# Kernel optimization log

Hardware: AMD Instinct MI355X
Metric: run time of the kernel (lower is better)

## Reference

```python
import jax, jax.numpy as jnp
import numpy as np

B, N, S, K = 8, 4096, 256, 128   # clouds, points/cloud, FPS samples (num_vote_test), neighbor cap
R = 0.2                           # ball-query radius
M = 45                            # FoldingNet grid side -> 45*45 = 2025 grid points


def _fps(pos):
    """Deterministic farthest point sampling of S points from pos [N,3] (start at index 0)."""
    n = pos.shape[0]
    big = jnp.finfo(pos.dtype).max

    def step(carry, _):
        mind, last = carry
        d = jnp.sum((pos - pos[last]) ** 2, axis=-1)
        mind = jnp.minimum(mind, d)
        nxt = jnp.argmax(mind).astype(jnp.int32)
        return (mind, nxt), nxt

    init = (jnp.full((n,), big, pos.dtype), jnp.int32(0))
    _, rest = jax.lax.scan(step, init, None, length=S - 1)
    return jnp.concatenate([jnp.zeros((1,), jnp.int32), rest])


def _forward(pos, Wt, bt, Wc1, bc1, Wc2, bc2, Wc3, bc3, We1, be1, We2, be2,
             Wf11, bf11, Wf12, bf12, Wf13, bf13, Wf21, bf21, Wf22, bf22, Wf23, bf23):
    lrelu = jax.nn.leaky_relu  # slope 0.01, matches torch LeakyReLU default
    # transformer: mlp([3,64]) -- BatchNorm at eval with default stats is identity
    x = lrelu(pos @ Wt + bt)                                  # [B,N,64]
    # FPS per cloud
    idx = jax.vmap(_fps)(pos)                                  # [B,S]
    new_pos = jnp.take_along_axis(pos, idx[..., None], axis=1)  # [B,S,3]
    # radius ball query: first K in-ball neighbors by index order (torch_cluster semantics)
    d2 = jnp.sum((new_pos[:, :, None, :] - pos[:, None, :, :]) ** 2, -1)  # [B,S,N]
    inball = d2 <= R * R
    keep = inball & (jnp.cumsum(inball, axis=-1) <= K)
    order = jnp.where(keep, jnp.arange(N)[None, None, :], N)
    nidx = jnp.sort(order, axis=-1)[..., :K]                   # [B,S,K]
    valid = nidx < N
    nsafe = jnp.minimum(nidx, N - 1)
    gather = jax.vmap(lambda a, i: a[i])
    xj = gather(x, nsafe)                                      # [B,S,K,64]
    pj = gather(pos, nsafe)                                    # [B,S,K,3]
    # PointConv: mlp(cat[x_j, pos_j - pos_i]) with max aggregation
    feat = jnp.concatenate([xj, pj - new_pos[:, :, None, :]], -1)  # [B,S,K,67]
    h = lrelu(feat @ Wc1 + bc1)
    h = lrelu(h @ Wc2 + bc2)
    h = lrelu(h @ Wc3 + bc3)                                   # [B,S,K,512]
    neg = jnp.finfo(h.dtype).min
    agg = jnp.max(jnp.where(valid[..., None], h, neg), axis=2)  # [B,S,512]
    # encoder mlp([515, 512, 2*bottleneck], last=True)
    e = lrelu(jnp.concatenate([agg, new_pos], -1) @ We1 + be1)
    e = e @ We2 + be2                                          # [B,S,2*bottleneck]
    mean, logvar = jnp.split(e, 2, axis=-1)
    std = jnp.exp(0.5 * logvar)
    # feature_selection (eval, rand=False): all S votes contribute; vote aggregation
    z = jnp.sum(mean / std, axis=1) / jnp.sum(1.0 / std, axis=1)  # [B,bottleneck]
    # FoldingNet decoder: 45x45 grid in [-0.3,0.3]^2, conv1x1 == last-dim linear
    g1 = np.linspace(-0.3, 0.3, M, dtype=np.float32)
    mg = np.meshgrid(g1, g1)
    grid = jnp.asarray(np.stack([mg[0].reshape(-1), mg[1].reshape(-1)], -1))  # [M*M,2]
    G = M * M
    code = jnp.broadcast_to(z[:, None, :], (z.shape[0], G, z.shape[1]))
    gb = jnp.broadcast_to(grid[None], (z.shape[0], G, 2))
    f = jnp.concatenate([code, gb], -1)                        # [B,G,bottleneck+2]
    f = jax.nn.relu(f @ Wf11 + bf11)
    f = jax.nn.relu(f @ Wf12 + bf12)
    f = f @ Wf13 + bf13                                        # [B,G,3]
    f2 = jnp.concatenate([code, f], -1)                        # [B,G,bottleneck+3]
    f2 = jax.nn.relu(f2 @ Wf21 + bf21)
    f2 = jax.nn.relu(f2 @ Wf22 + bf22)
    return f2 @ Wf23 + bf23                                    # [B,G,3]


_PARAM_SHAPES = [
    ("Wt", (3, 64)), ("bt", (64,)),
    ("Wc1", (67, 64)), ("bc1", (64,)),
    ("Wc2", (64, 128)), ("bc2", (128,)),
    ("Wc3", (128, 512)), ("bc3", (512,)),
    ("We1", (515, 512)), ("be1", (512,)),
    ("We2", (512, 2048)), ("be2", (2048,)),
    ("Wf11", (1026, 512)), ("bf11", (512,)),
    ("Wf12", (512, 512)), ("bf12", (512,)),
    ("Wf13", (512, 3)), ("bf13", (3,)),
    ("Wf21", (1027, 512)), ("bf21", (512,)),
    ("Wf22", (512, 512)), ("bf22", (512,)),
    ("Wf23", (512, 3)), ("bf23", (3,)),
]


def setup_inputs() -> dict:
    key = jax.random.key(0)
    inp = {"pos": jax.random.uniform(key, (B, N, 3), jnp.float32)}
    for i, (nm, sh) in enumerate(_PARAM_SHAPES):
        k = jax.random.fold_in(key, i + 1)
        fan_in = sh[0]
        inp[nm] = jax.random.normal(k, sh, jnp.float32) / np.sqrt(fan_in)
    return inp


def reference(pos, Wt, bt, Wc1, bc1, Wc2, bc2, Wc3, bc3, We1, be1, We2, be2,
              Wf11, bf11, Wf12, bf12, Wf13, bf13, Wf21, bf21, Wf22, bf22, Wf23, bf23):
    return _forward(pos, Wt, bt, Wc1, bc1, Wc2, bc2, Wc3, bc3, We1, be1, We2, be2,
                    Wf11, bf11, Wf12, bf12, Wf13, bf13, Wf21, bf21, Wf22, bf22, Wf23, bf23)
```

## Files before the change

### kernel.cpp

```cpp
#include <hip/hip_runtime.h>
#include <math.h>

#define BATCH 8
#define NPTS 4096
#define SSAMP 256
#define KNBR 128
#define GGRID 2025

typedef __attribute__((ext_vector_type(8))) short bf16x8;
typedef __attribute__((ext_vector_type(8))) unsigned short u16x8;
typedef __attribute__((ext_vector_type(4))) float f32x4;
#define MFMA16(a, b, c) __builtin_amdgcn_mfma_f32_16x16x32_bf16((a), (b), (c), 0, 0, 0)

__device__ __forceinline__ float lrelu01(float v) { return v > 0.f ? v : 0.01f * v; }
__device__ __forceinline__ unsigned short f2bf(float f) {
    unsigned u = __float_as_uint(f);
    unsigned r = (u + 0x7FFFu + ((u >> 16) & 1u)) >> 16;
    return (unsigned short)r;
}
__device__ __forceinline__ unsigned long long umax64(unsigned long long a, unsigned long long b) {
    return a > b ? a : b;
}

__global__ void preconv_kernel(const float* __restrict__ Wc1, const float* __restrict__ Wc2,
                               const float* __restrict__ Wc3, const float* __restrict__ We1,
                               const float* __restrict__ We2, const float* __restrict__ Wf12,
                               const float* __restrict__ Wf22,
                               unsigned short* __restrict__ W1T, unsigned short* __restrict__ W2T,
                               unsigned short* __restrict__ W3T, unsigned short* __restrict__ We1T,
                               unsigned short* __restrict__ We2T, unsigned short* __restrict__ Wf12T,
                               unsigned short* __restrict__ Wf22T) {
    int o = blockIdx.x * 256 + threadIdx.x;
    const int S1 = 6144, S2 = 8192, S3 = 65536, S4 = 294912, S5 = 1048576, S6 = 262144;
    if (o < S1) { int n = o / 96, k = o - n * 96; W1T[o] = f2bf(k < 67 ? Wc1[k * 64 + n] : 0.f); return; }
    o -= S1;
    if (o < S2) { int n = o >> 6, k = o & 63; W2T[o] = f2bf(Wc2[k * 128 + n]); return; }
    o -= S2;
    if (o < S3) { int n = o >> 7, k = o & 127; W3T[o] = f2bf(Wc3[k * 512 + n]); return; }
    o -= S3;
    if (o < S4) { int n = o / 576, k = o - n * 576; We1T[o] = f2bf(k < 515 ? We1[k * 512 + n] : 0.f); return; }
    o -= S4;
    if (o < S5) { int n = o >> 9, k = o & 511; We2T[o] = f2bf(We2[k * 2048 + n]); return; }
    o -= S5;
    if (o < S6) { int n = o >> 9, k = o & 511; Wf12T[o] = f2bf(Wf12[k * 512 + n]); return; }
    o -= S6;
    { int n = o >> 9, k = o & 511; Wf22T[o] = f2bf(Wf22[k * 512 + n]); }
}

__global__ void __launch_bounds__(256, 3) stage1_kernel(
    const float* __restrict__ pos, float* __restrict__ newpos, int* __restrict__ prog,
    const float* __restrict__ Wt, const float* __restrict__ bt,
    const unsigned short* __restrict__ W1T, const unsigned short* __restrict__ W2T,
    const unsigned short* __restrict__ W3T,
    const float* __restrict__ bc1, const float* __restrict__ bc2, const float* __restrict__ bc3,
    unsigned short* __restrict__ encin) {
    __shared__ __align__(16) unsigned char smem[53760];
    int blk = blockIdx.x, t = threadIdx.x;
    int wave = t >> 6, lane = t & 63;

    if (blk < 8) {
        float* pxs = (float*)smem;
        float* pys = (float*)(smem + 16384);
        float* pzs = (float*)(smem + 32768);
        float* npb = (float*)(smem + 49152);
        unsigned long long* rk = (unsigned long long*)(smem + 52224);
        int b = blk;
        const float* P = pos + (size_t)b * NPTS * 3;
        float* np = newpos + (size_t)b * SSAMP * 3;
        float px[16], py[16], pz[16], mind[16];
#pragma unroll
        for (int j = 0; j < 16; ++j) {
            int n = t + 256 * j;
            float X = P[n * 3 + 0], Y = P[n * 3 + 1], Z = P[n * 3 + 2];
            px[j] = X; py[j] = Y; pz[j] = Z;
            pxs[n] = X; pys[n] = Y; pzs[n] = Z;
            mind[j] = 3.402823466e+38f;
        }
        float cx = P[0], cy = P[1], cz = P[2];
        if (t == 0) { npb[0] = cx; npb[1] = cy; npb[2] = cz; }
        __syncthreads();
        for (int s = 1; s < SSAMP; ++s) {
            int p = s & 1;
            unsigned long long k[16];
#pragma unroll
            for (int j = 0; j < 16; ++j) {
                float dx = __fsub_rn(px[j], cx), dy = __fsub_rn(py[j], cy), dz = __fsub_rn(pz[j], cz);
                float d = __fadd_rn(__fadd_rn(__fmul_rn(dx, dx), __fmul_rn(dy, dy)), __fmul_rn(dz, dz));
                mind[j] = fminf(mind[j], d);
                k[j] = ((unsigned long long)__float_as_uint(mind[j]) << 32)
                     | (unsigned)~(unsigned)(t + 256 * j);
            }
#pragma unroll
            for (int st = 8; st > 0; st >>= 1)
#pragma unroll
                for (int j = 0; j < st; ++j) k[j] = umax64(k[j], k[j + st]);
            unsigned long long key = k[0];
            {
                unsigned long long a = __shfl_xor(key, 1, 64);
                unsigned long long b2 = __shfl_xor(key, 2, 64);
                unsigned long long c = __shfl_xor(key, 3, 64);
                key = umax64(umax64(key, a), umax64(b2, c));
                a = __shfl_xor(key, 4, 64);
                b2 = __shfl_xor(key, 8, 64);
                c = __shfl_xor(key, 12, 64);
                key = umax64(umax64(key, a), umax64(b2, c));
                a = __shfl_xor(key, 16, 64);
                b2 = __shfl_xor(key, 32, 64);
                c = __shfl_xor(key, 48, 64);
                key = umax64(umax64(key, a), umax64(b2, c));
            }
            if (lane == 0) rk[p * 4 + wave] = key;
            __syncthreads();
            unsigned long long k0 = rk[p * 4 + 0], k1 = rk[p * 4 + 1];
            unsigned long long k2 = rk[p * 4 + 2], k3 = rk[p * 4 + 3];
            unsigned long long bk = umax64(umax64(k0, k1), umax64(k2, k3));
            int nx = (int)(~(unsigned)(bk & 0xFFFFFFFFull));
            cx = pxs[nx]; cy = pys[nx]; cz = pzs[nx];
            if (t == 0) {
                npb[s * 3 + 0] = cx;
                npb[s * 3 + 1] = cy;
                npb[s * 3 + 2] = cz;
            }
            if ((s & 7) == 7) {
                if (t < 24) np[(s - 7) * 3 + t] = npb[(s - 7) * 3 + t];
                if (t == 0) {
                    __threadfence();
                    __hip_atomic_store(&prog[b], s, __ATOMIC_RELAXED, __HIP_MEMORY_SCOPE_AGENT);
                }
            }
        }
        return;
    }

    unsigned short* featl = (unsigned short*)smem;
    unsigned short* h2    = (unsigned short*)smem;
    unsigned short* h1    = (unsigned short*)(smem + 34816);
    float* mred = (float*)(smem + 34816);
    int*   vld  = (int*)(smem + 53248);
    int*   wl   = (int*)smem;
    int*   cnt  = (int*)(smem + 2048);
    float* wtb  = (float*)(smem + 26624);

    int cons = blk - 8;
    int s = cons >> 3, b = cons & 7;
    int bs = b * 256 + s;
    int quad = lane >> 4, l16 = lane & 15;

    if (t == 0) {
        while (__hip_atomic_load(&prog[b], __ATOMIC_RELAXED, __HIP_MEMORY_SCOPE_AGENT) < s)
            __builtin_amdgcn_s_sleep(16);
    }
    __syncthreads();
    __threadfence();
    float q0 = newpos[(size_t)bs * 3 + 0];
    float q1 = newpos[(size_t)bs * 3 + 1];
    float q2 = newpos[(size_t)bs * 3 + 2];

    const float* P = pos + (size_t)b * NPTS * 3;
    {
        int base = 0;
        for (int c = 0; c < 16 && base < KNBR; ++c) {
            int n = wave * 1024 + c * 64 + lane;
            float dx = __fsub_rn(P[n * 3 + 0], q0);
            float dy = __fsub_rn(P[n * 3 + 1], q1);
            float dz = __fsub_rn(P[n * 3 + 2], q2);
            float d2 = __fadd_rn(__fadd_rn(__fmul_rn(dx, dx), __fmul_rn(dy, dy)), __fmul_rn(dz, dz));
            bool in = (d2 <= 0.04f);
            unsigned long long mask = __ballot(in);
            if (in) {
                int p = base + __popcll(mask & ((1ull << lane) - 1ull));
                if (p < KNBR) wl[wave * 128 + p] = n;
            }
            base += __popcll(mask);
        }
        if (lane == 0) cnt[wave] = base < KNBR ? base : KNBR;
    }
    __syncthreads();
    {
        int c0 = cnt[0], c1 = cnt[1], c2 = cnt[2], c3 = cnt[3];
        if (t < 128) {
            int idx = -1, r = t;
            if (r < c0) idx = wl[r];
            else {
                r -= c0;
                if (r < c1) idx = wl[128 + r];
                else {
                    r -= c1;
                    if (r < c2) idx = wl[256 + r];
                    else { r -= c2; if (r < c3) idx = wl[384 + r]; }
                }
            }
            vld[t] = idx;
        }
        if (t < 192) wtb[t] = Wt[t];
        else wtb[t] = bt[t - 192];
    }
    __syncthreads();

    int vbits = 0;
#pragma unroll
    for (int i = 0; i < 2; ++i)
#pragma unroll
        for (int reg = 0; reg < 4; ++reg)
            if (vld[(2 * wave + i) * 16 + quad * 4 + reg] >= 0) vbits |= 1 << (i * 4 + reg);

    {
        int sr = t >> 1, sh = t & 1;
        int n = vld[sr];
        int ns = n < 0 ? 0 : n;
        const float* pp = pos + ((size_t)b * NPTS + ns) * 3;
        float p0 = pp[0], p1 = pp[1], p2 = pp[2];
        unsigned short* frow = &featl[sr * 104];
        u16x8 z8 = {0, 0, 0, 0, 0, 0, 0, 0};
        if (n >= 0) {
#pragma unroll
            for (int g = 0; g < 4; ++g) {
                u16x8 v8;
#pragma unroll
                for (int e = 0; e < 8; ++e) {
                    int c = sh * 32 + g * 8 + e;
                    float v = fmaf(p2, wtb[128 + c], fmaf(p1, wtb[64 + c], fmaf(p0, wtb[c], wtb[192 + c])));
                    v8[e] = (unsigned short)f2bf(lrelu01(v));
                }
                *(u16x8*)&frow[sh * 32 + g * 8] = v8;
            }
        } else {
#pragma unroll
            for (int g = 0; g < 4; ++g) *(u16x8*)&frow[sh * 32 + g * 8] = z8;
        }
        if (sh == 1) {
            u16x8 dv = z8;
            if (n >= 0) {
                dv[0] = (unsigned short)f2bf(__fsub_rn(p0, q0));
                dv[1] = (unsigned short)f2bf(__fsub_rn(p1, q1));
                dv[2] = (unsigned short)f2bf(__fsub_rn(p2, q2));
            }
            *(u16x8*)&frow[64] = dv;
            *(u16x8*)&frow[72] = z8;
            *(u16x8*)&frow[80] = z8;
            *(u16x8*)&frow[88] = z8;
        }
    }
    __syncthreads();

    {
        f32x4 acc[2][4];
#pragma unroll
        for (int i = 0; i < 2; ++i)
#pragma unroll
            for (int nt = 0; nt < 4; ++nt) acc[i][nt] = (f32x4){0.f, 0.f, 0.f, 0.f};
#pragma unroll
        for (int ks = 0; ks < 3; ++ks) {
            bf16x8 afr[2];
#pragma unroll
            for (int i = 0; i < 2; ++i)
                afr[i] = *(const bf16x8*)&featl[((2 * wave + i) * 16 + l16) * 104 + ks * 32 + quad * 8];
#pragma unroll
            for (int nt = 0; nt < 4; ++nt) {
                bf16x8 bfr = *(const bf16x8*)(W1T + (nt * 16 + l16) * 96 + ks * 32 + quad * 8);
                acc[0][nt] = MFMA16(afr[0], bfr, acc[0][nt]);
                acc[1][nt] = MFMA16(afr[1], bfr, acc[1][nt]);
            }
        }
#pragma unroll
        for (int i = 0; i < 2; ++i)
#pragma unroll
            for (int nt = 0; nt < 4; ++nt) {
                int col = nt * 16 + l16;
                float bias = bc1[col];
#pragma unroll
                for (int reg = 0; reg < 4; ++reg) {
                    int row = (2 * wave + i) * 16 + quad * 4 + reg;
                    h1[row * 72 + col] = f2bf(lrelu01(acc[i][nt][reg] + bias));
                }
            }
    }
    __syncthreads();

    {
        f32x4 acc[2][8];
#pragma unroll
        for (int i = 0; i < 2; ++i)
#pragma unroll
            for (int nt = 0; nt < 8; ++nt) acc[i][nt] = (f32x4){0.f, 0.f, 0.f, 0.f};
#pragma unroll
        for (int ks = 0; ks < 2; ++ks) {
            bf16x8 afr[2];
#pragma unroll
            for (int i = 0; i < 2; ++i)
                afr[i] = *(const bf16x8*)&h1[((2 * wave + i) * 16 + l16) * 72 + ks * 32 + quad * 8];
#pragma unroll
            for (int nt = 0; nt < 8; ++nt) {
                bf16x8 bfr = *(const bf16x8*)(W2T + (nt * 16 + l16) * 64 + ks * 32 + quad * 8);
                acc[0][nt] = MFMA16(afr[0], bfr, acc[0][nt]);
                acc[1][nt] = MFMA16(afr[1], bfr, acc[1][nt]);
            }
        }
        __syncthreads();
#pragma unroll
        for (int i = 0; i < 2; ++i)
#pragma unroll
            for (int nt = 0; nt < 8; ++nt) {
                int col = nt * 16 + l16;
                float bias = bc2[col];
#pragma unroll
                for (int reg = 0; reg < 4; ++reg) {
                    int row = (2 * wave + i) * 16 + quad * 4 + reg;
                    h2[row * 136 + col] = f2bf(lrelu01(acc[i][nt][reg] + bias));
                }
            }
    }
    __syncthreads();

    for (int c3 = 0; c3 < 4; ++c3) {
        f32x4 acc[2][8];
#pragma unroll
        for (int i = 0; i < 2; ++i)
#pragma unroll
            for (int nt = 0; nt < 8; ++nt) acc[i][nt] = (f32x4){0.f, 0.f, 0.f, 0.f};
#pragma unroll
        for (int ks = 0; ks < 4; ++ks) {
            bf16x8 afr[2];
#pragma unroll
            for (int i = 0; i < 2; ++i)
                afr[i] = *(const bf16x8*)&h2[((2 * wave + i) * 16 + l16) * 136 + ks * 32 + quad * 8];
#pragma unroll
            for (int nt = 0; nt < 8; ++nt) {
                bf16x8 bfr = *(const bf16x8*)(W3T + ((size_t)((c3 * 8 + nt) * 16 + l16)) * 128 + ks * 32 + quad * 8);
                acc[0][nt] = MFMA16(afr[0], bfr, acc[0][nt]);
                acc[1][nt] = MFMA16(afr[1], bfr, acc[1][nt]);
            }
        }
#pragma unroll
        for (int nt = 0; nt < 8; ++nt) {
            float vmax = -3.402823466e+38f;
#pragma unroll
            for (int i = 0; i < 2; ++i)
#pragma unroll
                for (int reg = 0; reg < 4; ++reg)
                    if (vbits & (1 << (i * 4 + reg))) vmax = fmaxf(vmax, acc[i][nt][reg]);
            vmax = fmaxf(vmax, __shfl_xor(vmax, 16));
            vmax = fmaxf(vmax, __shfl_xor(vmax, 32));
            if (lane < 16) mred[wave * 512 + (c3 * 8 + nt) * 16 + l16] = vmax;
        }
    }
    __syncthreads();
    unsigned short* erow = encin + (size_t)bs * 576;
    for (int c = t; c < 576; c += 256) {
        unsigned short v;
        if (c < 512) {
            float m4 = fmaxf(fmaxf(mred[c], mred[512 + c]), fmaxf(mred[1024 + c], mred[1536 + c]));
            v = f2bf(lrelu01(m4 + bc3[c]));
        } else if (c < 515) {
            v = f2bf(c == 512 ? q0 : (c == 513 ? q1 : q2));
        } else v = 0;
        erow[c] = v;
    }
}

__global__ void __launch_bounds__(256, 3) mfma_gemm(
    const unsigned short* __restrict__ A, const unsigned short* __restrict__ BT,
    const float* __restrict__ bias, float* __restrict__ outf, unsigned short* __restrict__ outh,
    int M, int Ka, int Ncols, int act) {
    __shared__ __align__(16) unsigned short As[128 * 72];
    int t = threadIdx.x;
    int wave = t >> 6, lane = t & 63, quad = lane >> 4, l16 = lane & 15;
    int row0 = blockIdx.x * 128, col0 = blockIdx.y * 128;
    f32x4 acc[2][8];
#pragma unroll
    for (int i = 0; i < 2; ++i)
#pragma unroll
        for (int nt = 0; nt < 8; ++nt) acc[i][nt] = (f32x4){0.f, 0.f, 0.f, 0.f};
    int nk = Ka >> 6;
    int sr = t >> 1, sh = t & 1;
    int grow = row0 + sr; if (grow > M - 1) grow = M - 1;
    const unsigned short* Arow = A + (size_t)grow * Ka + sh * 32;
    for (int ks = 0; ks < nk; ++ks) {
        u16x8 av[4];
#pragma unroll
        for (int j = 0; j < 4; ++j) av[j] = *(const u16x8*)(Arow + ks * 64 + j * 8);
        __syncthreads();
#pragma unroll
        for (int j = 0; j < 4; ++j) *(u16x8*)&As[sr * 72 + sh * 32 + j * 8] = av[j];
        __syncthreads();
#pragma unroll
        for (int ks2 = 0; ks2 < 2; ++ks2) {
            bf16x8 afr[2];
            afr[0] = *(const bf16x8*)&As[((2 * wave) * 16 + l16) * 72 + ks2 * 32 + quad * 8];
            afr[1] = *(const bf16x8*)&As[((2 * wave + 1) * 16 + l16) * 72 + ks2 * 32 + quad * 8];
#pragma unroll
            for (int nt = 0; nt < 8; ++nt) {
                bf16x8 bfr = *(const bf16x8*)(BT + (size_t)(col0 + nt * 16 + l16) * Ka + ks * 64 + ks2 * 32 + quad * 8);
                acc[0][nt] = MFMA16(afr[0], bfr, acc[0][nt]);
                acc[1][nt] = MFMA16(afr[1], bfr, acc[1][nt]);
            }
        }
    }
#pragma unroll
    for (int i = 0; i < 2; ++i)
#pragma unroll
        for (int nt = 0; nt < 8; ++nt) {
            int col = col0 + nt * 16 + l16;
            float bv = bias[col];
#pragma unroll
            for (int reg = 0; reg < 4; ++reg) {
                int row = row0 + (2 * wave + i) * 16 + quad * 4 + reg;
                if (row < M) {
                    float v = acc[i][nt][reg] + bv;
                    if (act == 1) v = fmaxf(v, 0.f);
                    else if (act == 2) v = lrelu01(v);
                    if (outh) outh[(size_t)row * Ncols + col] = f2bf(v);
                    else outf[(size_t)row * Ncols + col] = v;
                }
            }
        }
}

__global__ void __launch_bounds__(256) votes_kernel(const float* __restrict__ e, float* __restrict__ z) {
    __shared__ float red[8][32][2];
    int blk = blockIdx.x;
    int b = blk >> 5, c0 = (blk & 31) << 5;
    int t = threadIdx.x, c = t & 31, sg = t >> 5;
    const float* eb = e + (size_t)b * SSAMP * 2048;
    float num = 0.f, den = 0.f;
    for (int si = 0; si < 32; ++si) {
        int s = sg * 32 + si;
        float mean = eb[(size_t)s * 2048 + c0 + c];
        float lv = eb[(size_t)s * 2048 + 1024 + c0 + c];
        float sd = expf(0.5f * lv);
        num += mean / sd;
        den += 1.f / sd;
    }
    red[sg][c][0] = num; red[sg][c][1] = den;
    __syncthreads();
    if (sg == 0) {
        float n = 0.f, d = 0.f;
#pragma unroll
        for (int k = 0; k < 8; ++k) { n += red[k][c][0]; d += red[k][c][1]; }
        z[b * 1024 + c0 + c] = n / d;
    }
}

__global__ void __launch_bounds__(256) ukern(const float* __restrict__ z,
                                             const float* __restrict__ Wf11, const float* __restrict__ bf11,
                                             const float* __restrict__ Wf21, const float* __restrict__ bf21,
                                             float* __restrict__ u1, float* __restrict__ u2) {
    __shared__ float zt[1024 * 8];
    __shared__ float red[4][64][8];
    const float* W = blockIdx.y ? Wf21 : Wf11;
    const float* bias = blockIdx.y ? bf21 : bf11;
    float* u = blockIdx.y ? u2 : u1;
    int t = threadIdx.x;
#pragma unroll
    for (int i = 0; i < 32; ++i) {
        int o = t + i * 256;
        zt[(o & 1023) * 8 + (o >> 10)] = z[o];
    }
    __syncthreads();
    int c64 = t & 63, kc = t >> 6;
    int co = blockIdx.x * 64 + c64;
    float acc[8];
#pragma unroll
    for (int r = 0; r < 8; ++r) acc[r] = 0.f;
    for (int i = 0; i < 256; ++i) {
        int ci = kc * 256 + i;
        float w = W[(size_t)ci * 512 + co];
        const float4* zp = (const float4*)&zt[ci * 8];
        float4 z0 = zp[0], z1 = zp[1];
        acc[0] = fmaf(z0.x, w, acc[0]); acc[1] = fmaf(z0.y, w, acc[1]);
        acc[2] = fmaf(z0.z, w, acc[2]); acc[3] = fmaf(z0.w, w, acc[3]);
        acc[4] = fmaf(z1.x, w, acc[4]); acc[5] = fmaf(z1.y, w, acc[5]);
        acc[6] = fmaf(z1.z, w, acc[6]); acc[7] = fmaf(z1.w, w, acc[7]);
    }
#pragma unroll
    for (int r = 0; r < 8; ++r) red[kc][c64][r] = acc[r];
    __syncthreads();
    if (kc == 0) {
#pragma unroll
        for (int r = 0; r < 8; ++r) {
            float v = red[0][c64][r] + red[1][c64][r] + red[2][c64][r] + red[3][c64][r] + bias[co];
            u[r * 512 + co] = v;
        }
    }
}

__global__ void fold1_kernel(const float* __restrict__ u1, const float* __restrict__ Wf11,
                             unsigned short* __restrict__ f1) {
    int o = blockIdx.x * 256 + threadIdx.x;
    int co = o & 511;
    int rg = o >> 9;
    int b = rg / 2025;
    int g = rg - b * 2025;
    int i = g / 45, j = g - i * 45;
    float gx = (j == 44) ? 0.3f : (float)(-0.3 + j * (0.6 / 44.0));
    float gy = (i == 44) ? 0.3f : (float)(-0.3 + i * (0.6 / 44.0));
    float v = u1[(b << 9) + co];
    v = fmaf(gx, Wf11[1024 * 512 + co], v);
    v = fmaf(gy, Wf11[1025 * 512 + co], v);
    f1[o] = f2bf(fmaxf(v, 0.f));
}

__global__ void fold2_kernel(const float* __restrict__ u2, const float* __restrict__ Wf21,
                             const float* __restrict__ pts, unsigned short* __restrict__ f2) {
    int o = blockIdx.x * 256 + threadIdx.x;
    int co = o & 511;
    int rg = o >> 9;
    int b = rg / 2025;
    float p0 = pts[rg * 3 + 0], p1 = pts[rg * 3 + 1], p2 = pts[rg * 3 + 2];
    float v = u2[(b << 9) + co];
    v = fmaf(p0, Wf21[1024 * 512 + co], v);
    v = fmaf(p1, Wf21[1025 * 512 + co], v);
    v = fmaf(p2, Wf21[1026 * 512 + co], v);
    f2[o] = f2bf(fmaxf(v, 0.f));
}

__global__ void smallout_kernel(const unsigned short* __restrict__ H, const float* __restrict__ Wf,
                                const float* __restrict__ bf, float* __restrict__ out, int rows) {
    int rg = blockIdx.x * 256 + threadIdx.x;
    if (rg >= rows) return;
    const unsigned int* h = (const unsigned int*)(H + (size_t)rg * 512);
    float a0 = bf[0], a1 = bf[1], a2 = bf[2];
#pragma unroll 4
    for (int q = 0; q < 256; ++q) {
        unsigned int p = h[q];
        float e0 = __uint_as_float(p << 16);
        float e1 = __uint_as_float(p & 0xFFFF0000u);
        int k = q * 2;
        a0 = fmaf(e0, Wf[k * 3 + 0], a0);
        a1 = fmaf(e0, Wf[k * 3 + 1], a1);
        a2 = fmaf(e0, Wf[k * 3 + 2], a2);
        a0 = fmaf(e1, Wf[k * 3 + 3], a0);
        a1 = fmaf(e1, Wf[k * 3 + 4], a1);
        a2 = fmaf(e1, Wf[k * 3 + 5], a2);
    }
    out[rg * 3 + 0] = a0;
    out[rg * 3 + 1] = a1;
    out[rg * 3 + 2] = a2;
}

extern "C" void kernel_launch(void* const* d_in, const int* in_sizes, int n_in,
                              void* d_out, int out_size, void* d_ws, size_t ws_size,
                              hipStream_t stream) {
    const float* pos  = (const float*)d_in[0];
    const float* Wt   = (const float*)d_in[1];
    const float* bt   = (const float*)d_in[2];
    const float* Wc1  = (const float*)d_in[3];
    const float* bc1  = (const float*)d_in[4];
    const float* Wc2  = (const float*)d_in[5];
    const float* bc2  = (const float*)d_in[6];
    const float* Wc3  = (const float*)d_in[7];
    const float* bc3  = (const float*)d_in[8];
    const float* We1  = (const float*)d_in[9];
    const float* be1  = (const float*)d_in[10];
    const float* We2  = (const float*)d_in[11];
    const float* be2  = (const float*)d_in[12];
    const float* Wf11 = (const float*)d_in[13];
    const float* bf11 = (const float*)d_in[14];
    const float* Wf12 = (const float*)d_in[15];
    const float* bf12 = (const float*)d_in[16];
    const float* Wf13 = (const float*)d_in[17];
    const float* bf13 = (const float*)d_in[18];
    const float* Wf21 = (const float*)d_in[19];
    const float* bf21 = (const float*)d_in[20];
    const float* Wf22 = (const float*)d_in[21];
    const float* bf22 = (const float*)d_in[22];
    const float* Wf23 = (const float*)d_in[23];
    const float* bf23 = (const float*)d_in[24];
    float* out = (float*)d_out;

    float* wsf = (float*)d_ws;
    size_t off = 0;
    unsigned short* encinh= (unsigned short*)(wsf + off); off += 589824;
    unsigned short* e1h   = (unsigned short*)(wsf + off); off += 524288;
    float* e    = wsf + off; off += 4194304;
    unsigned short* f1h   = (unsigned short*)(wsf + off); off += 4147200;
    unsigned short* h12h  = (unsigned short*)(wsf + off); off += 4147200;
    float* zb   = wsf + off; off += 8192;
    float* u1   = wsf + off; off += 4096;
    float* u2   = wsf + off; off += 4096;
    float* pts  = wsf + off; off += 48600;
    float* newp = wsf + off; off += 6144;
    int*   prog = (int*)(wsf + off); off += 16;
    unsigned short* W1T   = (unsigned short*)(wsf + off); off += 3072;
    unsigned short* W2T   = (unsigned short*)(wsf + off); off += 4096;
    unsigned short* W3T   = (unsigned short*)(wsf + off); off += 32768;
    unsigned short* We1T  = (unsigned short*)(wsf + off); off += 147456;
    unsigned short* We2T  = (unsigned short*)(wsf + off); off += 524288;
    unsigned short* Wf12T = (unsigned short*)(wsf + off); off += 131072;
    unsigned short* Wf22T = (unsigned short*)(wsf + off); off += 131072;

    hipMemsetAsync(prog, 0xFF, 64, stream);
    preconv_kernel<<<7608, 256, 0, stream>>>(Wc1, Wc2, Wc3, We1, We2, Wf12, Wf22,
                                             W1T, W2T, W3T, We1T, We2T, Wf12T, Wf22T);
    stage1_kernel<<<2056, 256, 0, stream>>>(pos, newp, prog, Wt, bt, W1T, W2T, W3T,
                                            bc1, bc2, bc3, encinh);
    mfma_gemm<<<dim3(16, 4), 256, 0, stream>>>(encinh, We1T, be1, nullptr, e1h, 2048, 576, 512, 2);
    mfma_gemm<<<dim3(16, 16), 256, 0, stream>>>(e1h, We2T, be2, e, nullptr, 2048, 512, 2048, 0);
    votes_kernel<<<256, 256, 0, stream>>>(e, zb);
    ukern<<<dim3(8, 2), 256, 0, stream>>>(zb, Wf11, bf11, Wf21, bf21, u1, u2);
    fold1_kernel<<<32400, 256, 0, stream>>>(u1, Wf11, f1h);
    mfma_gemm<<<dim3(127, 4), 256, 0, stream>>>(f1h, Wf12T, bf12, nullptr, h12h, 16200, 512, 512, 1);
    smallout_kernel<<<64, 256, 0, stream>>>(h12h, Wf13, bf13, pts, 16200);
    fold2_kernel<<<32400, 256, 0, stream>>>(u2, Wf21, pts, f1h);
    mfma_gemm<<<dim3(127, 4), 256, 0, stream>>>(f1h, Wf22T, bf22, nullptr, h12h, 16200, 512, 512, 1);
    smallout_kernel<<<64, 256, 0, stream>>>(h12h, Wf23, bf23, out, 16200);
}
```

Baseline: 681.9 us.

## Fuse vote reduction into encoder GEMM and fold stages into single MFMA kernels

The second encoder GEMM now interleaves mean and log-variance columns in its weight layout so each lane pair can compute precision-weighted vote partial sums directly from accumulators. These sums go to global memory via atomics, which removes the fp32 intermediate and the separate votes kernel. Each folding stage (fold input build, 512x512 GEMM with ReLU, 512->3 projection) is fused into one kernel that builds the A tile on the fly and reduces the projection with shuffles, so the large bf16 intermediates are never written. The fold kernels launch only 127 blocks with a serial loop over four column chunks, which may leave the GPU underused. The atomics also make the vote sums order-nondeterministic.

```diff
diff --git a/kernel.cpp b/kernel.cpp
--- a/kernel.cpp
+++ b/kernel.cpp
@@ -40,7 +40,12 @@
     o -= S3;
     if (o < S4) { int n = o / 576, k = o - n * 576; We1T[o] = f2bf(k < 515 ? We1[k * 512 + n] : 0.f); return; }
     o -= S4;
-    if (o < S5) { int n = o >> 9, k = o & 511; We2T[o] = f2bf(We2[k * 2048 + n]); return; }
+    if (o < S5) {
+        int np = o >> 9, k = o & 511;
+        int src = (np & 1) ? 1024 + (np >> 1) : (np >> 1);
+        We2T[o] = f2bf(We2[(size_t)k * 2048 + src]);
+        return;
+    }
     o -= S5;
     if (o < S6) { int n = o >> 9, k = o & 511; Wf12T[o] = f2bf(Wf12[k * 512 + n]); return; }
     o -= S6;
@@ -360,7 +365,7 @@
 
 __global__ void __launch_bounds__(256, 3) mfma_gemm(
     const unsigned short* __restrict__ A, const unsigned short* __restrict__ BT,
-    const float* __restrict__ bias, float* __restrict__ outf, unsigned short* __restrict__ outh,
+    const float* __restrict__ bias, unsigned short* __restrict__ outh,
     int M, int Ka, int Ncols, int act) {
     __shared__ __align__(16) unsigned short As[128 * 72];
     int t = threadIdx.x;
@@ -409,39 +414,75 @@
                     float v = acc[i][nt][reg] + bv;
                     if (act == 1) v = fmaxf(v, 0.f);
                     else if (act == 2) v = lrelu01(v);
-                    if (outh) outh[(size_t)row * Ncols + col] = f2bf(v);
-                    else outf[(size_t)row * Ncols + col] = v;
-                }
-            }
-        }
-}
-
-__global__ void __launch_bounds__(256) votes_kernel(const float* __restrict__ e, float* __restrict__ z) {
-    __shared__ float red[8][32][2];
-    int blk = blockIdx.x;
-    int b = blk >> 5, c0 = (blk & 31) << 5;
-    int t = threadIdx.x, c = t & 31, sg = t >> 5;
-    const float* eb = e + (size_t)b * SSAMP * 2048;
-    float num = 0.f, den = 0.f;
-    for (int si = 0; si < 32; ++si) {
-        int s = sg * 32 + si;
-        float mean = eb[(size_t)s * 2048 + c0 + c];
-        float lv = eb[(size_t)s * 2048 + 1024 + c0 + c];
-        float sd = expf(0.5f * lv);
-        num += mean / sd;
-        den += 1.f / sd;
-    }
-    red[sg][c][0] = num; red[sg][c][1] = den;
-    __syncthreads();
-    if (sg == 0) {
-        float n = 0.f, d = 0.f;
-#pragma unroll
-        for (int k = 0; k < 8; ++k) { n += red[k][c][0]; d += red[k][c][1]; }
-        z[b * 1024 + c0 + c] = n / d;
-    }
-}
-
-__global__ void __launch_bounds__(256) ukern(const float* __restrict__ z,
+                    outh[(size_t)row * Ncols + col] = f2bf(v);
+                }
+            }
+        }
+}
+
+__global__ void __launch_bounds__(256, 3) e2v_kernel(
+    const unsigned short* __restrict__ A, const unsigned short* __restrict__ BT,
+    const float* __restrict__ be2, float* __restrict__ zacc) {
+    __shared__ __align__(16) unsigned short As[128 * 72];
+    int t = threadIdx.x;
+    int wave = t >> 6, lane = t & 63, quad = lane >> 4, l16 = lane & 15;
+    int row0 = blockIdx.x * 128, col0 = blockIdx.y * 128;
+    f32x4 acc[2][8];
+#pragma unroll
+    for (int i = 0; i < 2; ++i)
+#pragma unroll
+        for (int nt = 0; nt < 8; ++nt) acc[i][nt] = (f32x4){0.f, 0.f, 0.f, 0.f};
+    int sr = t >> 1, sh = t & 1;
+    const unsigned short* Arow = A + (size_t)(row0 + sr) * 512 + sh * 32;
+    for (int ks = 0; ks < 8; ++ks) {
+        u16x8 av[4];
+#pragma unroll
+        for (int j = 0; j < 4; ++j) av[j] = *(const u16x8*)(Arow + ks * 64 + j * 8);
+        __syncthreads();
+#pragma unroll
+        for (int j = 0; j < 4; ++j) *(u16x8*)&As[sr * 72 + sh * 32 + j * 8] = av[j];
+        __syncthreads();
+#pragma unroll
+        for (int ks2 = 0; ks2 < 2; ++ks2) {
+            bf16x8 afr[2];
+            afr[0] = *(const bf16x8*)&As[((2 * wave) * 16 + l16) * 72 + ks2 * 32 + quad * 8];
+            afr[1] = *(const bf16x8*)&As[((2 * wave + 1) * 16 + l16) * 72 + ks2 * 32 + quad * 8];
+#pragma unroll
+            for (int nt = 0; nt < 8; ++nt) {
+                bf16x8 bfr = *(const bf16x8*)(BT + (size_t)(col0 + nt * 16 + l16) * 512 + ks * 64 + ks2 * 32 + quad * 8);
+                acc[0][nt] = MFMA16(afr[0], bfr, acc[0][nt]);
+                acc[1][nt] = MFMA16(afr[1], bfr, acc[1][nt]);
+            }
+        }
+    }
+    int b = row0 >> 8;
+#pragma unroll
+    for (int nt = 0; nt < 8; ++nt) {
+        int colp = col0 + nt * 16 + l16;
+        int c2 = colp >> 1;
+        int srcc = (colp & 1) ? 1024 + c2 : c2;
+        float bv = be2[srcc];
+        float num = 0.f, den = 0.f;
+#pragma unroll
+        for (int i = 0; i < 2; ++i)
+#pragma unroll
+            for (int reg = 0; reg < 4; ++reg) {
+                float val = acc[i][nt][reg] + bv;
+                float par = __shfl_xor(val, 1, 64);
+                float d = expf(-0.5f * par);
+                num += val * d;
+                den += d;
+            }
+        num += __shfl_xor(num, 16, 64); den += __shfl_xor(den, 16, 64);
+        num += __shfl_xor(num, 32, 64); den += __shfl_xor(den, 32, 64);
+        if (quad == 0 && !(l16 & 1)) {
+            atomicAdd(&zacc[((b << 10) + c2) * 2 + 0], num);
+            atomicAdd(&zacc[((b << 10) + c2) * 2 + 1], den);
+        }
+    }
+}
+
+__global__ void __launch_bounds__(256) ukern(const float* __restrict__ zacc,
                                              const float* __restrict__ Wf11, const float* __restrict__ bf11,
                                              const float* __restrict__ Wf21, const float* __restrict__ bf21,
                                              float* __restrict__ u1, float* __restrict__ u2) {
@@ -451,10 +492,12 @@
     const float* bias = blockIdx.y ? bf21 : bf11;
     float* u = blockIdx.y ? u2 : u1;
     int t = threadIdx.x;
+    const float2* za = (const float2*)zacc;
 #pragma unroll
     for (int i = 0; i < 32; ++i) {
         int o = t + i * 256;
-        zt[(o & 1023) * 8 + (o >> 10)] = z[o];
+        float2 nd = za[o];
+        zt[(o & 1023) * 8 + (o >> 10)] = nd.x / nd.y;
     }
     __syncthreads();
     int c64 = t & 63, kc = t >> 6;
@@ -484,58 +527,128 @@
     }
 }
 
-__global__ void fold1_kernel(const float* __restrict__ u1, const float* __restrict__ Wf11,
-                             unsigned short* __restrict__ f1) {
-    int o = blockIdx.x * 256 + threadIdx.x;
-    int co = o & 511;
-    int rg = o >> 9;
-    int b = rg / 2025;
-    int g = rg - b * 2025;
-    int i = g / 45, j = g - i * 45;
-    float gx = (j == 44) ? 0.3f : (float)(-0.3 + j * (0.6 / 44.0));
-    float gy = (i == 44) ? 0.3f : (float)(-0.3 + i * (0.6 / 44.0));
-    float v = u1[(b << 9) + co];
-    v = fmaf(gx, Wf11[1024 * 512 + co], v);
-    v = fmaf(gy, Wf11[1025 * 512 + co], v);
-    f1[o] = f2bf(fmaxf(v, 0.f));
-}
-
-__global__ void fold2_kernel(const float* __restrict__ u2, const float* __restrict__ Wf21,
-                             const float* __restrict__ pts, unsigned short* __restrict__ f2) {
-    int o = blockIdx.x * 256 + threadIdx.x;
-    int co = o & 511;
-    int rg = o >> 9;
-    int b = rg / 2025;
-    float p0 = pts[rg * 3 + 0], p1 = pts[rg * 3 + 1], p2 = pts[rg * 3 + 2];
-    float v = u2[(b << 9) + co];
-    v = fmaf(p0, Wf21[1024 * 512 + co], v);
-    v = fmaf(p1, Wf21[1025 * 512 + co], v);
-    v = fmaf(p2, Wf21[1026 * 512 + co], v);
-    f2[o] = f2bf(fmaxf(v, 0.f));
-}
-
-__global__ void smallout_kernel(const unsigned short* __restrict__ H, const float* __restrict__ Wf,
-                                const float* __restrict__ bf, float* __restrict__ out, int rows) {
-    int rg = blockIdx.x * 256 + threadIdx.x;
-    if (rg >= rows) return;
-    const unsigned int* h = (const unsigned int*)(H + (size_t)rg * 512);
-    float a0 = bf[0], a1 = bf[1], a2 = bf[2];
-#pragma unroll 4
-    for (int q = 0; q < 256; ++q) {
-        unsigned int p = h[q];
-        float e0 = __uint_as_float(p << 16);
-        float e1 = __uint_as_float(p & 0xFFFF0000u);
-        int k = q * 2;
-        a0 = fmaf(e0, Wf[k * 3 + 0], a0);
-        a1 = fmaf(e0, Wf[k * 3 + 1], a1);
-        a2 = fmaf(e0, Wf[k * 3 + 2], a2);
-        a0 = fmaf(e1, Wf[k * 3 + 3], a0);
-        a1 = fmaf(e1, Wf[k * 3 + 4], a1);
-        a2 = fmaf(e1, Wf[k * 3 + 5], a2);
-    }
-    out[rg * 3 + 0] = a0;
-    out[rg * 3 + 1] = a1;
-    out[rg * 3 + 2] = a2;
+__global__ void __launch_bounds__(256, 3) foldfuse_kernel(
+    const float* __restrict__ u, const float* __restrict__ Wfold, int nExtra, int mode,
+    const unsigned short* __restrict__ WT, const float* __restrict__ bmid,
+    const float* __restrict__ wout, const float* __restrict__ bout,
+    const float* __restrict__ pts_in, float* __restrict__ outv) {
+    __shared__ __align__(16) unsigned short As[128 * 72];
+    __shared__ float sW[3][512];
+    __shared__ float sU[2][512];
+    __shared__ float sP[512 * 3];
+    __shared__ float sB[512];
+    __shared__ float sRC[128][4];
+    int t = threadIdx.x, wave = t >> 6, lane = t & 63, quad = lane >> 4, l16 = lane & 15;
+    int row0 = blockIdx.x * 128;
+    int b0 = row0 / 2025;
+
+    for (int idx = t; idx < 1536; idx += 256) {
+        int r = idx >> 9, c = idx & 511;
+        sW[r][c] = (r < nExtra) ? Wfold[(size_t)(1024 + r) * 512 + c] : 0.f;
+    }
+    for (int idx = t; idx < 1536; idx += 256) sP[idx] = wout[idx];
+    for (int idx = t; idx < 1024; idx += 256) {
+        int rb = idx >> 9;
+        int bb = b0 + rb; if (bb > 7) bb = 7;
+        sU[rb][idx & 511] = u[bb * 512 + (idx & 511)];
+    }
+    for (int idx = t; idx < 512; idx += 256) sB[idx] = bmid[idx];
+    if (t < 128) {
+        int rg = row0 + t; if (rg > 16199) rg = 16199;
+        int b = rg / 2025, g = rg - b * 2025;
+        if (mode == 0) {
+            int i = g / 45, j = g - i * 45;
+            sRC[t][0] = (j == 44) ? 0.3f : (float)(-0.3 + j * (0.6 / 44.0));
+            sRC[t][1] = (i == 44) ? 0.3f : (float)(-0.3 + i * (0.6 / 44.0));
+            sRC[t][2] = 0.f;
+        } else {
+            sRC[t][0] = pts_in[rg * 3 + 0];
+            sRC[t][1] = pts_in[rg * 3 + 1];
+            sRC[t][2] = pts_in[rg * 3 + 2];
+        }
+        sRC[t][3] = __int_as_float(b - b0);
+    }
+    __syncthreads();
+
+    float proj[2][4][3];
+#pragma unroll
+    for (int i = 0; i < 2; ++i)
+#pragma unroll
+        for (int r = 0; r < 4; ++r) { proj[i][r][0] = 0.f; proj[i][r][1] = 0.f; proj[i][r][2] = 0.f; }
+
+    int sr = t >> 1, sh = t & 1;
+    for (int cc = 0; cc < 4; ++cc) {
+        f32x4 acc[2][8];
+#pragma unroll
+        for (int i = 0; i < 2; ++i)
+#pragma unroll
+            for (int nt = 0; nt < 8; ++nt) acc[i][nt] = (f32x4){0.f, 0.f, 0.f, 0.f};
+        for (int ks = 0; ks < 8; ++ks) {
+            __syncthreads();
+            {
+                int ubi = __float_as_int(sRC[sr][3]);
+                float r0 = sRC[sr][0], r1 = sRC[sr][1], r2 = sRC[sr][2];
+                const float* up = sU[ubi];
+                int cbase = ks * 64 + sh * 32;
+#pragma unroll
+                for (int g2 = 0; g2 < 16; ++g2) {
+                    int c = cbase + g2 * 2;
+                    float v0 = fmaf(r2, sW[2][c],     fmaf(r1, sW[1][c],     fmaf(r0, sW[0][c],     up[c])));
+                    float v1 = fmaf(r2, sW[2][c + 1], fmaf(r1, sW[1][c + 1], fmaf(r0, sW[0][c + 1], up[c + 1])));
+                    unsigned pk = (unsigned)f2bf(fmaxf(v0, 0.f)) | ((unsigned)f2bf(fmaxf(v1, 0.f)) << 16);
+                    *(unsigned*)&As[sr * 72 + sh * 32 + g2 * 2] = pk;
+                }
+            }
+            __syncthreads();
+#pragma unroll
+            for (int ks2 = 0; ks2 < 2; ++ks2) {
+                bf16x8 afr0 = *(const bf16x8*)&As[((2 * wave) * 16 + l16) * 72 + ks2 * 32 + quad * 8];
+                bf16x8 afr1 = *(const bf16x8*)&As[((2 * wave + 1) * 16 + l16) * 72 + ks2 * 32 + quad * 8];
+#pragma unroll
+                for (int nt = 0; nt < 8; ++nt) {
+                    bf16x8 bfr = *(const bf16x8*)(WT + (size_t)(cc * 128 + nt * 16 + l16) * 512 + ks * 64 + ks2 * 32 + quad * 8);
+                    acc[0][nt] = MFMA16(afr0, bfr, acc[0][nt]);
+                    acc[1][nt] = MFMA16(afr1, bfr, acc[1][nt]);
+                }
+            }
+        }
+#pragma unroll
+        for (int i = 0; i < 2; ++i)
+#pragma unroll
+            for (int nt = 0; nt < 8; ++nt) {
+                int col = cc * 128 + nt * 16 + l16;
+                float bv = sB[col];
+                float w0 = sP[col * 3 + 0], w1 = sP[col * 3 + 1], w2 = sP[col * 3 + 2];
+#pragma unroll
+                for (int reg = 0; reg < 4; ++reg) {
+                    float h = fmaxf(acc[i][nt][reg] + bv, 0.f);
+                    proj[i][reg][0] = fmaf(h, w0, proj[i][reg][0]);
+                    proj[i][reg][1] = fmaf(h, w1, proj[i][reg][1]);
+                    proj[i][reg][2] = fmaf(h, w2, proj[i][reg][2]);
+                }
+            }
+    }
+    float o0 = bout[0], o1 = bout[1], o2 = bout[2];
+#pragma unroll
+    for (int i = 0; i < 2; ++i)
+#pragma unroll
+        for (int reg = 0; reg < 4; ++reg) {
+            float p0 = proj[i][reg][0], p1 = proj[i][reg][1], p2 = proj[i][reg][2];
+#pragma unroll
+            for (int m = 1; m < 16; m <<= 1) {
+                p0 += __shfl_xor(p0, m, 64);
+                p1 += __shfl_xor(p1, m, 64);
+                p2 += __shfl_xor(p2, m, 64);
+            }
+            if (l16 == 0) {
+                int row = row0 + (2 * wave + i) * 16 + quad * 4 + reg;
+                if (row < 16200) {
+                    outv[row * 3 + 0] = p0 + o0;
+                    outv[row * 3 + 1] = p1 + o1;
+                    outv[row * 3 + 2] = p2 + o2;
+                }
+            }
+        }
 }
 
 extern "C" void kernel_launch(void* const* d_in, const int* in_sizes, int n_in,
@@ -572,10 +685,7 @@
     size_t off = 0;
     unsigned short* encinh= (unsigned short*)(wsf + off); off += 589824;
     unsigned short* e1h   = (unsigned short*)(wsf + off); off += 524288;
-    float* e    = wsf + off; off += 4194304;
-    unsigned short* f1h   = (unsigned short*)(wsf + off); off += 4147200;
-    unsigned short* h12h  = (unsigned short*)(wsf + off); off += 4147200;
-    float* zb   = wsf + off; off += 8192;
+    float* zacc = wsf + off; off += 16384;
     float* u1   = wsf + off; off += 4096;
     float* u2   = wsf + off; off += 4096;
     float* pts  = wsf + off; off += 48600;
@@ -590,18 +700,14 @@
     unsigned short* Wf22T = (unsigned short*)(wsf + off); off += 131072;
 
     hipMemsetAsync(prog, 0xFF, 64, stream);
+    hipMemsetAsync(zacc, 0x00, 16384 * 4, stream);
     preconv_kernel<<<7608, 256, 0, stream>>>(Wc1, Wc2, Wc3, We1, We2, Wf12, Wf22,
                                              W1T, W2T, W3T, We1T, We2T, Wf12T, Wf22T);
     stage1_kernel<<<2056, 256, 0, stream>>>(pos, newp, prog, Wt, bt, W1T, W2T, W3T,
                                             bc1, bc2, bc3, encinh);
-    mfma_gemm<<<dim3(16, 4), 256, 0, stream>>>(encinh, We1T, be1, nullptr, e1h, 2048, 576, 512, 2);
-    mfma_gemm<<<dim3(16, 16), 256, 0, stream>>>(e1h, We2T, be2, e, nullptr, 2048, 512, 2048, 0);
-    votes_kernel<<<256, 256, 0, stream>>>(e, zb);
-    ukern<<<dim3(8, 2), 256, 0, stream>>>(zb, Wf11, bf11, Wf21, bf21, u1, u2);
-    fold1_kernel<<<32400, 256, 0, stream>>>(u1, Wf11, f1h);
-    mfma_gemm<<<dim3(127, 4), 256, 0, stream>>>(f1h, Wf12T, bf12, nullptr, h12h, 16200, 512, 512, 1);
-    smallout_kernel<<<64, 256, 0, stream>>>(h12h, Wf13, bf13, pts, 16200);
-    fold2_kernel<<<32400, 256, 0, stream>>>(u2, Wf21, pts, f1h);
-    mfma_gemm<<<dim3(127, 4), 256, 0, stream>>>(f1h, Wf22T, bf22, nullptr, h12h, 16200, 512, 512, 1);
-    smallout_kernel<<<64, 256, 0, stream>>>(h12h, Wf23, bf23, out, 16200);
-}
+    mfma_gemm<<<dim3(16, 4), 256, 0, stream>>>(encinh, We1T, be1, e1h, 2048, 576, 512, 2);
+    e2v_kernel<<<dim3(16, 16), 256, 0, stream>>>(e1h, We2T, be2, zacc);
+    ukern<<<dim3(8, 2), 256, 0, stream>>>(zacc, Wf11, bf11, Wf21, bf21, u1, u2);
+    foldfuse_kernel<<<127, 256, 0, stream>>>(u1, Wf11, 2, 0, Wf12T, bf12, Wf13, bf13, pts, pts);
+    foldfuse_kernel<<<127, 256, 0, stream>>>(u2, Wf21, 3, 1, Wf22T, bf22, Wf23, bf23, pts, out);
+}
```

New measurement: 697.1 us. +2.2%, slower.
